# Optimization experiments

Hardware: AMD Instinct MI355X
Metric: run time of the kernel (lower is better)

## Reference

```python
import jax, jax.numpy as jnp
import numpy as np

N_POINTS = 262144
FEAT_DIM = 512
NUM_LABELS = 200
NUM_NEG = 8
IGNORE_LABEL = 255
POS_THRESH = 0.0
NEG_THRESH = 0.85
NEG_WEIGHT = 1.0
EPS = 1e-7


def setup_inputs() -> dict:
    key = jax.random.key(0)
    k1, k2, k3, k4 = jax.random.split(key, 4)
    features = jax.random.normal(k1, (N_POINTS, FEAT_DIM), dtype=jnp.float32)
    labels = jax.random.randint(k2, (N_POINTS,), 0, NUM_LABELS, dtype=jnp.int64)
    anchor_feats = jax.random.normal(k3, (NUM_LABELS, FEAT_DIM), dtype=jnp.float32)
    # uniform negatives over all labels != own label (clip_uniform_sampling=True):
    # sample r in [0, NUM_LABELS-1) and shift past the own label.
    r = jax.random.randint(k4, (N_POINTS, NUM_NEG), 0, NUM_LABELS - 1, dtype=jnp.int64)
    neg_inds = r + (r >= labels[:, None]).astype(jnp.int64)
    return {"features": features, "labels": labels,
            "anchor_feats": anchor_feats, "neg_inds": neg_inds}


def reference(features, labels, anchor_feats, neg_inds):
    # l2 feat_dist via ||a||^2 - 2 a.b + ||b||^2 against the small anchor table,
    # avoiding the [N, K, D] gathered intermediate of the torch code (same math).
    dots = features @ anchor_feats.T                      # [N, L]
    f2 = jnp.sum(features * features, axis=-1)            # [N]
    a2 = jnp.sum(anchor_feats * anchor_feats, axis=-1)    # [L]

    # positive: own-label anchor (1 sample -> mean over 1 is identity)
    pos_dot = jnp.take_along_axis(dots, labels[:, None], axis=1)[:, 0]
    pos_d2 = f2 - 2.0 * pos_dot + a2[labels]
    pos_dist = jnp.sqrt(jnp.maximum(pos_d2, 0.0) + EPS)   # [N]

    # negatives: K sampled anchors per point
    neg_dot = jnp.take_along_axis(dots, neg_inds, axis=1)  # [N, K]
    neg_d2 = f2[:, None] - 2.0 * neg_dot + a2[neg_inds]
    neg_dist = jnp.sqrt(jnp.maximum(neg_d2, 0.0) + EPS).mean(axis=1)  # [N]

    valid = labels != IGNORE_LABEL
    pos_dist = jnp.where(valid, pos_dist, 0.0)
    neg_dist = jnp.where(valid, neg_dist, 0.0)

    pos_loss = jax.nn.relu(pos_dist - POS_THRESH)
    neg_loss = jax.nn.relu(NEG_THRESH - neg_dist)
    loss = pos_loss.mean() + neg_loss.mean() * NEG_WEIGHT
    return loss, pos_loss, neg_loss
```

## Files before the change

kernel.cpp:

```cpp
#include <hip/hip_runtime.h>

constexpr int   N_POINTS     = 262144;
constexpr int   FEAT_DIM     = 512;
constexpr int   NUM_NEG      = 8;
constexpr int   IGNORE_LABEL = 255;
constexpr float NEG_THRESH   = 0.85f;
constexpr float POS_THRESH   = 0.0f;
constexpr float EPS          = 1e-7f;


__global__ void zero_ws_kernel(float* ws) {
    ws[0] = 0.f;
    ws[1] = 0.f;
}

__global__ __launch_bounds__(256, 4) void ccl_main_kernel(
    const float* __restrict__ features,
    const int*   __restrict__ labels,
    const float* __restrict__ anchors,
    const int*   __restrict__ neg_inds,
    float*       __restrict__ out,
    float*       __restrict__ ws)
{
    const int lane   = threadIdx.x & 63;
    const int wid    = threadIdx.x >> 6;
    const int gwave  = blockIdx.x * 4 + wid;
    const int nwaves = gridDim.x * 4;

    float* pos_out = out + 1;
    float* neg_out = out + 1 + N_POINTS;

    float sum_pos = 0.f, sum_neg = 0.f;

    for (int p = gwave; p < N_POINTS; p += nwaves) {
        const float4* frow = (const float4*)(features + (size_t)p * FEAT_DIM);
        const float4 fa = frow[lane];
        const float4 fb = frow[lane + 64];

        const int  lab   = labels[p];
        const bool valid = (lab != IGNORE_LABEL);

        int idx[9];
        idx[0] = valid ? lab : 0;
#pragma unroll
        for (int k = 0; k < NUM_NEG; ++k)
            idx[k + 1] = neg_inds[(size_t)p * NUM_NEG + k];

        float d2[9];
#pragma unroll
        for (int k = 0; k < 9; ++k) {
            const float4* arow = (const float4*)(anchors + (size_t)idx[k] * FEAT_DIM);
            const float4 aa = arow[lane];
            const float4 ab = arow[lane + 64];
            float s, dx;
            dx = fa.x - aa.x; s  = dx * dx;
            dx = fa.y - aa.y; s  = fmaf(dx, dx, s);
            dx = fa.z - aa.z; s  = fmaf(dx, dx, s);
            dx = fa.w - aa.w; s  = fmaf(dx, dx, s);
            dx = fb.x - ab.x; s  = fmaf(dx, dx, s);
            dx = fb.y - ab.y; s  = fmaf(dx, dx, s);
            dx = fb.z - ab.z; s  = fmaf(dx, dx, s);
            dx = fb.w - ab.w; s  = fmaf(dx, dx, s);
            d2[k] = s;
        }

#pragma unroll
        for (int k = 0; k < 9; ++k) {
            float v = d2[k];
#pragma unroll
            for (int off = 32; off > 0; off >>= 1)
                v += __shfl_xor(v, off, 64);
            d2[k] = v;
        }

        float pos_dist = sqrtf(d2[0] + EPS);
        float acc = 0.f;
#pragma unroll
        for (int k = 1; k < 9; ++k)
            acc += sqrtf(d2[k] + EPS);
        float neg_dist = acc * (1.0f / NUM_NEG);

        if (!valid) { pos_dist = 0.f; neg_dist = 0.f; }

        const float pos_loss = fmaxf(pos_dist - POS_THRESH, 0.f);
        const float neg_loss = fmaxf(NEG_THRESH - neg_dist, 0.f);

        if (lane == 0) {
            pos_out[p] = pos_loss;
            neg_out[p] = neg_loss;
            sum_pos += pos_loss;
            sum_neg += neg_loss;
        }
    }

    __shared__ float sp[4], sn[4];
    if (lane == 0) { sp[wid] = sum_pos; sn[wid] = sum_neg; }
    __syncthreads();
    if (threadIdx.x == 0) {
        atomicAdd(&ws[0], sp[0] + sp[1] + sp[2] + sp[3]);
        atomicAdd(&ws[1], sn[0] + sn[1] + sn[2] + sn[3]);
    }
}

__global__ void finalize_kernel(const float* __restrict__ ws,
                                float* __restrict__ out) {
    out[0] = (ws[0] + ws[1]) * (1.0f / (float)N_POINTS);
}

extern "C" void kernel_launch(void* const* d_in, const int* in_sizes, int n_in,
                              void* d_out, int out_size, void* d_ws, size_t ws_size,
                              hipStream_t stream) {
    const float* features = (const float*)d_in[0];
    const int*   labels   = (const int*)  d_in[1];
    const float* anchors  = (const float*)d_in[2];
    const int*   neg_inds = (const int*)  d_in[3];
    float* out = (float*)d_out;
    float* ws  = (float*)d_ws;

    zero_ws_kernel<<<1, 1, 0, stream>>>(ws);

    ccl_main_kernel<<<4096, 256, 0, stream>>>(features, labels, anchors,
                                              neg_inds, out, ws);

    finalize_kernel<<<1, 1, 0, stream>>>(ws, out);
}
```

Baseline: 878.1 us.

## Process one point per 16-lane group and use dot-product distance expansion

Replaces the grid-stride loop, where one wave handles one point, with a launch that maps each point to a 16-lane sub-group, so 16 points are processed per block and many more loads are in flight. Distances are now computed as ||f||^2 - 2 f·a + ||a||^2, with anchor squared norms precomputed by a new small kernel, which cuts per-element work and shortens the shuffle reductions to 4 steps. The cost is one extra launch, many more blocks, one atomic pair per 16 points, and higher register use for the 8 float4 feature values held per lane.

```diff
diff --git a/kernel.cpp b/kernel.cpp
--- a/kernel.cpp
+++ b/kernel.cpp
@@ -2,6 +2,7 @@
 
 constexpr int   N_POINTS     = 262144;
 constexpr int   FEAT_DIM     = 512;
+constexpr int   NUM_LABELS   = 200;
 constexpr int   NUM_NEG      = 8;
 constexpr int   IGNORE_LABEL = 255;
 constexpr float NEG_THRESH   = 0.85f;
@@ -14,91 +15,115 @@
     ws[1] = 0.f;
 }
 
+__global__ __launch_bounds__(256) void a2_kernel(const float* __restrict__ anchors,
+                                                 float* __restrict__ a2) {
+    const int w    = (blockIdx.x * 256 + threadIdx.x) >> 6;
+    const int lane = threadIdx.x & 63;
+    if (w >= NUM_LABELS) return;
+    const float4* row = (const float4*)(anchors + (size_t)w * FEAT_DIM);
+    const float4 a = row[lane];
+    const float4 b = row[lane + 64];
+    float s = a.x*a.x + a.y*a.y + a.z*a.z + a.w*a.w
+            + b.x*b.x + b.y*b.y + b.z*b.z + b.w*b.w;
+#pragma unroll
+    for (int off = 32; off > 0; off >>= 1) s += __shfl_xor(s, off, 64);
+    if (lane == 0) a2[w] = s;
+}
+
 __global__ __launch_bounds__(256, 4) void ccl_main_kernel(
     const float* __restrict__ features,
     const int*   __restrict__ labels,
     const float* __restrict__ anchors,
     const int*   __restrict__ neg_inds,
+    const float* __restrict__ a2,
     float*       __restrict__ out,
     float*       __restrict__ ws)
 {
-    const int lane   = threadIdx.x & 63;
-    const int wid    = threadIdx.x >> 6;
-    const int gwave  = blockIdx.x * 4 + wid;
-    const int nwaves = gridDim.x * 4;
+    const int tid   = threadIdx.x;
+    const int qlane = tid & 15;
+    const int quart = tid >> 4;
+    const int p     = blockIdx.x * 16 + quart;
 
     float* pos_out = out + 1;
     float* neg_out = out + 1 + N_POINTS;
 
-    float sum_pos = 0.f, sum_neg = 0.f;
+    const int  lab   = labels[p];
+    const bool valid = (lab != IGNORE_LABEL);
+    int idx[9];
+    idx[0] = valid ? lab : 0;
+#pragma unroll
+    for (int k = 0; k < NUM_NEG; ++k)
+        idx[k + 1] = neg_inds[(size_t)p * NUM_NEG + k];
 
-    for (int p = gwave; p < N_POINTS; p += nwaves) {
-        const float4* frow = (const float4*)(features + (size_t)p * FEAT_DIM);
-        const float4 fa = frow[lane];
-        const float4 fb = frow[lane + 64];
+    const float4* frow = (const float4*)(features + (size_t)p * FEAT_DIM);
+    float4 f[8];
+#pragma unroll
+    for (int j = 0; j < 8; ++j) f[j] = frow[qlane + 16 * j];
 
-        const int  lab   = labels[p];
-        const bool valid = (lab != IGNORE_LABEL);
+    float f2 = 0.f;
+#pragma unroll
+    for (int j = 0; j < 8; ++j) {
+        f2 = fmaf(f[j].x, f[j].x, f2);
+        f2 = fmaf(f[j].y, f[j].y, f2);
+        f2 = fmaf(f[j].z, f[j].z, f2);
+        f2 = fmaf(f[j].w, f[j].w, f2);
+    }
 
-        int idx[9];
-        idx[0] = valid ? lab : 0;
+    float dot[9];
 #pragma unroll
-        for (int k = 0; k < NUM_NEG; ++k)
-            idx[k + 1] = neg_inds[(size_t)p * NUM_NEG + k];
-
-        float d2[9];
+    for (int k = 0; k < 9; ++k) {
+        const float4* arow = (const float4*)(anchors + (size_t)idx[k] * FEAT_DIM);
+        float s = 0.f;
 #pragma unroll
-        for (int k = 0; k < 9; ++k) {
-            const float4* arow = (const float4*)(anchors + (size_t)idx[k] * FEAT_DIM);
-            const float4 aa = arow[lane];
-            const float4 ab = arow[lane + 64];
-            float s, dx;
-            dx = fa.x - aa.x; s  = dx * dx;
-            dx = fa.y - aa.y; s  = fmaf(dx, dx, s);
-            dx = fa.z - aa.z; s  = fmaf(dx, dx, s);
-            dx = fa.w - aa.w; s  = fmaf(dx, dx, s);
-            dx = fb.x - ab.x; s  = fmaf(dx, dx, s);
-            dx = fb.y - ab.y; s  = fmaf(dx, dx, s);
-            dx = fb.z - ab.z; s  = fmaf(dx, dx, s);
-            dx = fb.w - ab.w; s  = fmaf(dx, dx, s);
-            d2[k] = s;
+        for (int j = 0; j < 8; ++j) {
+            const float4 a = arow[qlane + 16 * j];
+            s = fmaf(f[j].x, a.x, s);
+            s = fmaf(f[j].y, a.y, s);
+            s = fmaf(f[j].z, a.z, s);
+            s = fmaf(f[j].w, a.w, s);
         }
+        dot[k] = s;
+    }
 
 #pragma unroll
-        for (int k = 0; k < 9; ++k) {
-            float v = d2[k];
+    for (int off = 8; off > 0; off >>= 1) f2 += __shfl_xor(f2, off, 16);
 #pragma unroll
-            for (int off = 32; off > 0; off >>= 1)
-                v += __shfl_xor(v, off, 64);
-            d2[k] = v;
-        }
-
-        float pos_dist = sqrtf(d2[0] + EPS);
-        float acc = 0.f;
+    for (int k = 0; k < 9; ++k) {
+        float v = dot[k];
 #pragma unroll
-        for (int k = 1; k < 9; ++k)
-            acc += sqrtf(d2[k] + EPS);
-        float neg_dist = acc * (1.0f / NUM_NEG);
-
-        if (!valid) { pos_dist = 0.f; neg_dist = 0.f; }
-
-        const float pos_loss = fmaxf(pos_dist - POS_THRESH, 0.f);
-        const float neg_loss = fmaxf(NEG_THRESH - neg_dist, 0.f);
-
-        if (lane == 0) {
-            pos_out[p] = pos_loss;
-            neg_out[p] = neg_loss;
-            sum_pos += pos_loss;
-            sum_neg += neg_loss;
-        }
+        for (int off = 8; off > 0; off >>= 1) v += __shfl_xor(v, off, 16);
+        dot[k] = v;
     }
 
-    __shared__ float sp[4], sn[4];
-    if (lane == 0) { sp[wid] = sum_pos; sn[wid] = sum_neg; }
+    const float pos_d2   = f2 - 2.f * dot[0] + a2[idx[0]];
+    float       pos_dist = sqrtf(fmaxf(pos_d2, 0.f) + EPS);
+    float acc = 0.f;
+#pragma unroll
+    for (int k = 1; k < 9; ++k) {
+        const float d2 = f2 - 2.f * dot[k] + a2[idx[k]];
+        acc += sqrtf(fmaxf(d2, 0.f) + EPS);
+    }
+    float neg_dist = acc * (1.0f / NUM_NEG);
+
+    if (!valid) { pos_dist = 0.f; neg_dist = 0.f; }
+
+    const float pos_loss = fmaxf(pos_dist - POS_THRESH, 0.f);
+    const float neg_loss = fmaxf(NEG_THRESH - neg_dist, 0.f);
+
+    __shared__ float sp[16], sn[16];
+    if (qlane == 0) {
+        pos_out[p] = pos_loss;
+        neg_out[p] = neg_loss;
+        sp[quart]  = pos_loss;
+        sn[quart]  = neg_loss;
+    }
     __syncthreads();
-    if (threadIdx.x == 0) {
-        atomicAdd(&ws[0], sp[0] + sp[1] + sp[2] + sp[3]);
-        atomicAdd(&ws[1], sn[0] + sn[1] + sn[2] + sn[3]);
+    if (tid == 0) {
+        float s0 = 0.f, s1 = 0.f;
+#pragma unroll
+        for (int i = 0; i < 16; ++i) { s0 += sp[i]; s1 += sn[i]; }
+        atomicAdd(&ws[0], s0);
+        atomicAdd(&ws[1], s1);
     }
 }
 
@@ -116,11 +141,14 @@
     const int*   neg_inds = (const int*)  d_in[3];
     float* out = (float*)d_out;
     float* ws  = (float*)d_ws;
+    float* a2  = ws + 2;
 
     zero_ws_kernel<<<1, 1, 0, stream>>>(ws);
 
-    ccl_main_kernel<<<4096, 256, 0, stream>>>(features, labels, anchors,
-                                              neg_inds, out, ws);
+    a2_kernel<<<50, 256, 0, stream>>>(anchors, a2);
+
+    ccl_main_kernel<<<N_POINTS / 16, 256, 0, stream>>>(features, labels, anchors,
+                                                       neg_inds, a2, out, ws);
 
     finalize_kernel<<<1, 1, 0, stream>>>(ws, out);
 }
```

Result: slower. 2.995 ms (+241.0%).
